# Kernel tuning notes

Measured on AMD Instinct MI355X. Metric: run time of the kernel, lower is better.

## Reference

```python
import jax, jax.numpy as jnp
import numpy as np
from jax import lax
from jax.scipy.special import logsumexp

B, T, H, L = 64, 512, 768, 9


def setup_inputs() -> dict:
    key = jax.random.key(0)
    k1, k2, k3, k4, k5 = jax.random.split(key, 5)
    hidden = jax.random.normal(k1, (B, T, H), dtype=jnp.float32)
    W = jax.random.normal(k2, (L, H), dtype=jnp.float32) * 0.02
    b = jnp.zeros((L,), dtype=jnp.float32)
    transitions = jax.random.normal(k3, (L, L), dtype=jnp.float32) * 0.1
    lengths = jax.random.randint(k4, (B,), T // 2, T + 1)
    seq_mask = jnp.arange(T)[None, :] < lengths[:, None]          # [B,T] bool
    labels = jax.random.randint(k5, (B, T), 0, L).astype(jnp.int32)
    labels = jnp.where(seq_mask, labels, -100).astype(jnp.int32)   # -100 = ignore
    attention_mask = seq_mask.astype(jnp.int32)
    return {"hidden": hidden, "W": W, "b": b, "transitions": transitions,
            "labels": labels, "attention_mask": attention_mask}


def _crf_nll(logits, tags, transitions, mask):
    # numerator: joint score of the gold path (no start/end transitions)
    maskf = mask.astype(logits.dtype)
    emit = jnp.take_along_axis(logits, tags[..., None], axis=2)[..., 0]   # [B,T]
    emit_score = (emit * maskf).sum(-1)
    trans = transitions[tags[:, :-1], tags[:, 1:]]                        # [B,T-1]
    trans_score = (trans * maskf[:, 1:]).sum(-1)
    numerator = emit_score + trans_score
    # denominator: forward algorithm (log-sum-exp recurrence over time)
    def step(alpha, xs):
        logit_t, mask_t = xs                                   # [B,L], [B]
        inner = alpha[:, :, None] + transitions[None, :, :] + logit_t[:, None, :]
        new = logsumexp(inner, axis=1)
        return jnp.where(mask_t[:, None], new, alpha), None
    alpha0 = logits[:, 0]                                      # mask[:,0] assumed True
    alpha, _ = lax.scan(step, alpha0,
                        (jnp.transpose(logits[:, 1:], (1, 0, 2)), mask[:, 1:].T))
    denominator = logsumexp(alpha, axis=-1)
    return -(numerator - denominator).sum()


def _viterbi(logits, transitions, mask):
    num_tags = transitions.shape[0]
    identity_bp = jnp.broadcast_to(jnp.arange(num_tags)[None, :], logits.shape[:1] + (num_tags,))

    def vstep(vscore, xs):
        logit_t, mask_t = xs
        inner = vscore[:, :, None] + transitions[None, :, :]   # [B,L_prev,L_cur]
        bp = jnp.argmax(inner, axis=1)                         # [B,L]
        new = jnp.max(inner, axis=1) + logit_t
        vscore = jnp.where(mask_t[:, None], new, vscore)
        bp = jnp.where(mask_t[:, None], bp, identity_bp)       # carry tag through pad
        return vscore, bp

    vscore0 = logits[:, 0]
    vscore, bps = lax.scan(vstep, vscore0,
                           (jnp.transpose(logits[:, 1:], (1, 0, 2)), mask[:, 1:].T))
    last_tag = jnp.argmax(vscore, axis=-1)                     # [B]

    def btstep(tag, bp_t):
        prev = jnp.take_along_axis(bp_t, tag[:, None], axis=1)[:, 0]
        return prev, tag

    first_tag, tags_rest = lax.scan(btstep, last_tag, bps, reverse=True)  # ys[t]=tag_{t+1}
    return jnp.concatenate([first_tag[:, None], tags_rest.T], axis=1)     # [B,T]


def reference(hidden, W, b, transitions, labels, attention_mask):
    mask = (attention_mask != 0) & (labels != -100)            # create_combined_mask
    logits = jnp.einsum('bth,lh->btl', hidden, W) + b          # classifier (dropout=eval)
    tags = jnp.where(labels == -100, 0, labels)                # adjust_labels_for_crf
    loss = _crf_nll(logits, tags, transitions, mask)           # -log_likelihood (summed)
    vtags = _viterbi(logits, transitions, mask)                # [B,T]
    # pad_predictions: prepend -100, shift right, -100 outside the masked span
    bsz = hidden.shape[0]
    neg = jnp.full((bsz, 1), -100, dtype=jnp.int32)
    shifted = jnp.concatenate([neg, vtags[:, :-1].astype(jnp.int32)], axis=1)
    valid = jnp.concatenate([jnp.zeros((bsz, 1), bool), mask[:, :-1]], axis=1)
    predictions = jnp.where(valid, shifted, -100)
    return loss, predictions
```

## Files before the change

kernel.cpp:

```cpp
#include <hip/hip_runtime.h>

#define BATCH 64
#define TLEN  512
#define HDIM  768
#define LTAGS 9

#define WS_LOGD 0
#define WS_VM   2359296
#define WS_AM   5308416
#define WS_NUM  5971968

__global__ __launch_bounds__(256) void logits_kernel(
    const float* __restrict__ hidden, const float* __restrict__ W,
    const float* __restrict__ bvec, double* __restrict__ logitsD)
{
    __shared__ float sW[LTAGS * HDIM];
    __shared__ float sb[LTAGS];
    const int tid = threadIdx.x;
    for (int i = tid; i < LTAGS * HDIM; i += 256) sW[i] = W[i];
    if (tid < LTAGS) sb[tid] = bvec[tid];
    __syncthreads();

    const int lane = tid & 63;
    const int wave = tid >> 6;
    const int sub  = lane & 7;
    const int rg   = lane >> 3;

    const int rowBase = blockIdx.x * 64 + wave * 16;
    const int r0 = rowBase + rg;
    const int r1 = rowBase + rg + 8;
    const float* h0p = hidden + (size_t)r0 * HDIM;
    const float* h1p = hidden + (size_t)r1 * HDIM;

    double acc0[LTAGS], acc1[LTAGS];
    #pragma unroll
    for (int l = 0; l < LTAGS; ++l) { acc0[l] = 0.0; acc1[l] = 0.0; }

    #pragma unroll 2
    for (int i = 0; i < 24; ++i) {
        const int off = i * 32 + sub * 4;
        const float4 h0 = *(const float4*)(h0p + off);
        const float4 h1 = *(const float4*)(h1p + off);
        #pragma unroll
        for (int l = 0; l < LTAGS; ++l) {
            const float4 w = *(const float4*)&sW[l * HDIM + off];
            float d0 = h0.x * w.x;
            d0 = fmaf(h0.y, w.y, d0); d0 = fmaf(h0.z, w.z, d0); d0 = fmaf(h0.w, w.w, d0);
            float d1 = h1.x * w.x;
            d1 = fmaf(h1.y, w.y, d1); d1 = fmaf(h1.z, w.z, d1); d1 = fmaf(h1.w, w.w, d1);
            acc0[l] += (double)d0;
            acc1[l] += (double)d1;
        }
    }
    #pragma unroll
    for (int l = 0; l < LTAGS; ++l) {
        double v0 = acc0[l], v1 = acc1[l];
        #pragma unroll
        for (int off = 4; off > 0; off >>= 1) {
            v0 += __shfl_down(v0, off);
            v1 += __shfl_down(v1, off);
        }
        acc0[l] = v0; acc1[l] = v1;
    }
    if (sub == 0) {
        #pragma unroll
        for (int l = 0; l < LTAGS; ++l) {
            logitsD[(size_t)r0 * LTAGS + l] = acc0[l] + (double)sb[l];
            logitsD[(size_t)r1 * LTAGS + l] = acc1[l] + (double)sb[l];
        }
    }
}

__global__ __launch_bounds__(256) void chunk_kernel(
    const float* __restrict__ trans, const int* __restrict__ labels,
    const int* __restrict__ att, const double* __restrict__ logitsD,
    double* __restrict__ wsVM, float* __restrict__ wsAM,
    double* __restrict__ wsNum, float* __restrict__ out)
{
    __shared__ __align__(16) double sT64[90];
    __shared__ __align__(16) float  sE32[108];
    const int tid = threadIdx.x;
    if (tid < 81) {
        const int k = tid / 9, j = tid - 9 * k;
        float tv = trans[tid];
        sT64[k * 10 + j] = (double)tv;
        sE32[k * 12 + j] = __expf(tv);
    }
    if (blockIdx.x == 0 && tid == 0) out[0] = 0.f;
    __syncthreads();

    const int blk = blockIdx.x;
    if (blk < 144) {
        const int gid = blk * 256 + tid;
        const int b   = gid / 576;
        const int rem = gid - b * 576;
        const int c   = rem / 9;
        const int i   = rem - c * 9;

        double M[LTAGS];
        #pragma unroll
        for (int j = 0; j < LTAGS; ++j) M[j] = (i == j) ? 0.0 : -1e300;

        const double* lrow = logitsD + ((size_t)b * TLEN + (c * 8 + 1)) * LTAGS;
        const int* lab = labels + b * TLEN;
        const int* am  = att + b * TLEN;
        const int t0 = c * 8 + 1;

        double lg[LTAGS], lgN[LTAGS];
        #pragma unroll
        for (int j = 0; j < LTAGS; ++j) lg[j] = lrow[j];
        bool mk = (am[t0] != 0) && (lab[t0] != -100);

        for (int s = 0; s < 8; ++s) {
            bool mkN = false;
            const int tn = t0 + s + 1;
            if (s < 7 && tn <= TLEN - 1) {
                const double* ln = lrow + (s + 1) * LTAGS;
                #pragma unroll
                for (int j = 0; j < LTAGS; ++j) lgN[j] = ln[j];
                mkN = (am[tn] != 0) && (lab[tn] != -100);
            }
            double nw[LTAGS];
            #pragma unroll
            for (int k = 0; k < LTAGS; ++k) {
                const double2* r = (const double2*)&sT64[k * 10];
                const double2 r01 = r[0], r23 = r[1], r45 = r[2], r67 = r[3];
                const double r8 = sT64[k * 10 + 8];
                const double mk64 = M[k];
                if (k == 0) {
                    nw[0] = mk64 + r01.x; nw[1] = mk64 + r01.y;
                    nw[2] = mk64 + r23.x; nw[3] = mk64 + r23.y;
                    nw[4] = mk64 + r45.x; nw[5] = mk64 + r45.y;
                    nw[6] = mk64 + r67.x; nw[7] = mk64 + r67.y;
                    nw[8] = mk64 + r8;
                } else {
                    nw[0] = fmax(nw[0], mk64 + r01.x); nw[1] = fmax(nw[1], mk64 + r01.y);
                    nw[2] = fmax(nw[2], mk64 + r23.x); nw[3] = fmax(nw[3], mk64 + r23.y);
                    nw[4] = fmax(nw[4], mk64 + r45.x); nw[5] = fmax(nw[5], mk64 + r45.y);
                    nw[6] = fmax(nw[6], mk64 + r67.x); nw[7] = fmax(nw[7], mk64 + r67.y);
                    nw[8] = fmax(nw[8], mk64 + r8);
                }
            }
            #pragma unroll
            for (int j = 0; j < LTAGS; ++j) {
                M[j] = mk ? (nw[j] + lg[j]) : M[j];
                lg[j] = lgN[j];
            }
            mk = mkN;
        }
        double* dst = wsVM + ((size_t)b * 64 + c) * 90 + (size_t)i * 10;
        #pragma unroll
        for (int j = 0; j < LTAGS; ++j) dst[j] = M[j];
    } else if (blk < 216) {
        const int gid = (blk - 144) * 256 + tid;
        const int b   = gid / 288;
        const int rem = gid - b * 288;
        const int c   = rem / 9;
        const int i   = rem - c * 9;

        float M[LTAGS];
        #pragma unroll
        for (int j = 0; j < LTAGS; ++j) M[j] = (i == j) ? 0.f : -1e30f;

        const double* lrow = logitsD + ((size_t)b * TLEN + (c * 16 + 1)) * LTAGS;
        const int* lab = labels + b * TLEN;
        const int* am  = att + b * TLEN;
        const int t0 = c * 16 + 1;

        float lg[LTAGS], lgN[LTAGS];
        #pragma unroll
        for (int j = 0; j < LTAGS; ++j) lg[j] = (float)lrow[j];
        bool mk = (am[t0] != 0) && (lab[t0] != -100);

        for (int s = 0; s < 16; ++s) {
            bool mkN = false;
            const int tn = t0 + s + 1;
            if (s < 15 && tn <= TLEN - 1) {
                const double* ln = lrow + (s + 1) * LTAGS;
                #pragma unroll
                for (int j = 0; j < LTAGS; ++j) lgN[j] = (float)ln[j];
                mkN = (am[tn] != 0) && (lab[tn] != -100);
            }
            float m = M[0];
            #pragma unroll
            for (int k = 1; k < LTAGS; ++k) m = fmaxf(m, M[k]);
            float P[LTAGS];
            #pragma unroll
            for (int k = 0; k < LTAGS; ++k) P[k] = __expf(M[k] - m);
            float sa[LTAGS];
            #pragma unroll
            for (int k = 0; k < LTAGS; ++k) {
                const float4* r = (const float4*)&sE32[k * 12];
                const float4 f03 = r[0], f47 = r[1];
                const float f8 = sE32[k * 12 + 8];
                const float pk = P[k];
                if (k == 0) {
                    sa[0] = pk * f03.x; sa[1] = pk * f03.y; sa[2] = pk * f03.z; sa[3] = pk * f03.w;
                    sa[4] = pk * f47.x; sa[5] = pk * f47.y; sa[6] = pk * f47.z; sa[7] = pk * f47.w;
                    sa[8] = pk * f8;
                } else {
                    sa[0] = fmaf(pk, f03.x, sa[0]); sa[1] = fmaf(pk, f03.y, sa[1]);
                    sa[2] = fmaf(pk, f03.z, sa[2]); sa[3] = fmaf(pk, f03.w, sa[3]);
                    sa[4] = fmaf(pk, f47.x, sa[4]); sa[5] = fmaf(pk, f47.y, sa[5]);
                    sa[6] = fmaf(pk, f47.z, sa[6]); sa[7] = fmaf(pk, f47.w, sa[7]);
                    sa[8] = fmaf(pk, f8,    sa[8]);
                }
            }
            #pragma unroll
            for (int j = 0; j < LTAGS; ++j) {
                float nwj = m + __logf(sa[j]) + lg[j];
                M[j] = mk ? nwj : M[j];
                lg[j] = lgN[j];
            }
            mk = mkN;
        }
        float* dst = wsAM + (((size_t)b * 32 + c) * LTAGS + i) * LTAGS;
        #pragma unroll
        for (int j = 0; j < LTAGS; ++j) dst[j] = M[j];
    } else {
        const int bb   = (blk - 216) * 4 + (tid >> 6);
        const int lane = tid & 63;
        const int* lab = labels + bb * TLEN;
        const int* am  = att + bb * TLEN;
        const double* lrowb = logitsD + (size_t)bb * TLEN * LTAGS;
        double part = 0.0;
        #pragma unroll
        for (int k = 0; k < 8; ++k) {
            const int t = lane + k * 64;
            int lv = lab[t], av = am[t];
            bool mkc = (av != 0) && (lv != -100);
            int tg = (lv == -100) ? 0 : lv;
            if (mkc) part += lrowb[(size_t)t * LTAGS + tg];
            if (t < TLEN - 1) {
                int lv2 = lab[t + 1], av2 = am[t + 1];
                bool mk2 = (av2 != 0) && (lv2 != -100);
                int tg2 = (lv2 == -100) ? 0 : lv2;
                if (mk2) part += sT64[tg * 10 + tg2];
            }
        }
        #pragma unroll
        for (int off = 32; off > 0; off >>= 1) part += __shfl_down(part, off);
        if (lane == 0) wsNum[bb] = part;
    }
}

__global__ __launch_bounds__(128) void crf2_kernel(
    const float* __restrict__ trans, const int* __restrict__ labels,
    const int* __restrict__ att, const double* __restrict__ logitsD,
    const double* __restrict__ wsVM, const float* __restrict__ wsAM,
    const double* __restrict__ wsNum, float* __restrict__ out)
{
    __shared__ __align__(16) double sVM[64 * 90];
    __shared__ __align__(16) float  sAM[32 * 81];
    __shared__ __align__(16) double sU[720];
    __shared__ __align__(16) double sT64[90];
    __shared__ unsigned char sMk[513];
    __shared__ int sTagB[65];
    __shared__ double sDen;

    const int b = blockIdx.x, tid = threadIdx.x;
    const int wave = tid >> 6, lane = tid & 63;
    const unsigned long long IDMAP = 0x876543210ull;

    const double2* gVM = (const double2*)(wsVM + (size_t)b * 5760);
    double2* sVM2 = (double2*)sVM;
    for (int i = tid; i < 2880; i += 128) sVM2[i] = gVM[i];
    const float4* gAM = (const float4*)(wsAM + (size_t)b * 2592);
    float4* sAM4 = (float4*)sAM;
    for (int i = tid; i < 648; i += 128) sAM4[i] = gAM[i];

    const int* lab = labels + b * TLEN;
    const int* am  = att + b * TLEN;
    for (int t = tid; t < TLEN; t += 128) {
        int lv = lab[t], av = am[t];
        sMk[t] = (av != 0 && lv != -100) ? 1 : 0;
    }
    if (tid == 0) sMk[TLEN] = 0;
    if (tid < 81) {
        const int k = tid / 9, j = tid - 9 * k;
        sT64[k * 10 + j] = (double)trans[tid];
    }
    __syncthreads();

    double* sSM = sU;
    if (tid < 72) {
        const int g = tid / 9, i = tid - 9 * g;
        double P[LTAGS];
        {
            const double* row = &sVM[(g * 8) * 90 + i * 10];
            #pragma unroll
            for (int j = 0; j < LTAGS; ++j) P[j] = row[j];
        }
        for (int m = g * 8 + 1; m < g * 8 + 8; ++m) {
            double np[LTAGS];
            #pragma unroll
            for (int k = 0; k < LTAGS; ++k) {
                const double2* r = (const double2*)&sVM[m * 90 + k * 10];
                const double2 r01 = r[0], r23 = r[1], r45 = r[2], r67 = r[3];
                const double r8 = sVM[m * 90 + k * 10 + 8];
                const double pk = P[k];
                if (k == 0) {
                    np[0] = pk + r01.x; np[1] = pk + r01.y;
                    np[2] = pk + r23.x; np[3] = pk + r23.y;
                    np[4] = pk + r45.x; np[5] = pk + r45.y;
                    np[6] = pk + r67.x; np[7] = pk + r67.y;
                    np[8] = pk + r8;
                } else {
                    np[0] = fmax(np[0], pk + r01.x); np[1] = fmax(np[1], pk + r01.y);
                    np[2] = fmax(np[2], pk + r23.x); np[3] = fmax(np[3], pk + r23.y);
                    np[4] = fmax(np[4], pk + r45.x); np[5] = fmax(np[5], pk + r45.y);
                    np[6] = fmax(np[6], pk + r67.x); np[7] = fmax(np[7], pk + r67.y);
                    np[8] = fmax(np[8], pk + r8);
                }
            }
            #pragma unroll
            for (int j = 0; j < LTAGS; ++j) P[j] = np[j];
        }
        double* dst = &sSM[g * 90 + i * 10];
        #pragma unroll
        for (int j = 0; j < LTAGS; ++j) dst[j] = P[j];
    }
    __syncthreads();

    unsigned long long* sBPp = (unsigned long long*)sU;
    unsigned long long S = IDMAP;
    int lastTag = 0;

    if (wave == 0) {
        const int c = lane;
        const int myg = c >> 3;
        double v[LTAGS], vS[LTAGS];
        #pragma unroll
        for (int j = 0; j < LTAGS; ++j) v[j] = logitsD[(size_t)b * TLEN * LTAGS + j];

        #pragma unroll
        for (int g = 0; g < 8; ++g) {
            if (g == myg) {
                #pragma unroll
                for (int j = 0; j < LTAGS; ++j) vS[j] = v[j];
            }
            double nv[LTAGS];
            #pragma unroll
            for (int k = 0; k < LTAGS; ++k) {
                const double2* r = (const double2*)&sSM[g * 90 + k * 10];
                const double2 r01 = r[0], r23 = r[1], r45 = r[2], r67 = r[3];
                const double r8 = sSM[g * 90 + k * 10 + 8];
                const double vk = v[k];
                if (k == 0) {
                    nv[0] = vk + r01.x; nv[1] = vk + r01.y;
                    nv[2] = vk + r23.x; nv[3] = vk + r23.y;
                    nv[4] = vk + r45.x; nv[5] = vk + r45.y;
                    nv[6] = vk + r67.x; nv[7] = vk + r67.y;
                    nv[8] = vk + r8;
                } else {
                    nv[0] = fmax(nv[0], vk + r01.x); nv[1] = fmax(nv[1], vk + r01.y);
                    nv[2] = fmax(nv[2], vk + r23.x); nv[3] = fmax(nv[3], vk + r23.y);
                    nv[4] = fmax(nv[4], vk + r45.x); nv[5] = fmax(nv[5], vk + r45.y);
                    nv[6] = fmax(nv[6], vk + r67.x); nv[7] = fmax(nv[7], vk + r67.y);
                    nv[8] = fmax(nv[8], vk + r8);
                }
            }
            #pragma unroll
            for (int j = 0; j < LTAGS; ++j) v[j] = nv[j];
        }
        {
            int bi = 0; double bv = v[0];
            #pragma unroll
            for (int i = 1; i < LTAGS; ++i) if (v[i] > bv) { bv = v[i]; bi = i; }
            lastTag = bi;
        }

        const int nCat = c & 7;
        for (int it = 0; it < nCat; ++it) {
            const int m = (c & ~7) + it;
            double nv[LTAGS];
            #pragma unroll
            for (int k = 0; k < LTAGS; ++k) {
                const double2* r = (const double2*)&sVM[m * 90 + k * 10];
                const double2 r01 = r[0], r23 = r[1], r45 = r[2], r67 = r[3];
                const double r8 = sVM[m * 90 + k * 10 + 8];
                const double vk = vS[k];
                if (k == 0) {
                    nv[0] = vk + r01.x; nv[1] = vk + r01.y;
                    nv[2] = vk + r23.x; nv[3] = vk + r23.y;
                    nv[4] = vk + r45.x; nv[5] = vk + r45.y;
                    nv[6] = vk + r67.x; nv[7] = vk + r67.y;
                    nv[8] = vk + r8;
                } else {
                    nv[0] = fmax(nv[0], vk + r01.x); nv[1] = fmax(nv[1], vk + r01.y);
                    nv[2] = fmax(nv[2], vk + r23.x); nv[3] = fmax(nv[3], vk + r23.y);
                    nv[4] = fmax(nv[4], vk + r45.x); nv[5] = fmax(nv[5], vk + r45.y);
                    nv[6] = fmax(nv[6], vk + r67.x); nv[7] = fmax(nv[7], vk + r67.y);
                    nv[8] = fmax(nv[8], vk + r8);
                }
            }
            #pragma unroll
            for (int j = 0; j < LTAGS; ++j) vS[j] = nv[j];
        }

        const double* lrow = logitsD + ((size_t)b * TLEN + (c * 8 + 1)) * LTAGS;
        double lg[LTAGS], lgN[LTAGS];
        #pragma unroll
        for (int j = 0; j < LTAGS; ++j) lg[j] = lrow[j];

        for (int s = 0; s < 8; ++s) {
            const int t = c * 8 + 1 + s;
            if (s < 7 && t + 1 <= TLEN - 1) {
                const double* ln = lrow + (s + 1) * LTAGS;
                #pragma unroll
                for (int j = 0; j < LTAGS; ++j) lgN[j] = ln[j];
            }
            const bool mk = (sMk[t] != 0);
            double bst[LTAGS];
            int bi[LTAGS];
            #pragma unroll
            for (int k = 0; k < LTAGS; ++k) {
                const double2* r = (const double2*)&sT64[k * 10];
                const double2 r01 = r[0], r23 = r[1], r45 = r[2], r67 = r[3];
                const double r8 = sT64[k * 10 + 8];
                const double vk = vS[k];
                double cnd[LTAGS];
                cnd[0] = vk + r01.x; cnd[1] = vk + r01.y;
                cnd[2] = vk + r23.x; cnd[3] = vk + r23.y;
                cnd[4] = vk + r45.x; cnd[5] = vk + r45.y;
                cnd[6] = vk + r67.x; cnd[7] = vk + r67.y;
                cnd[8] = vk + r8;
                if (k == 0) {
                    #pragma unroll
                    for (int j = 0; j < LTAGS; ++j) { bst[j] = cnd[j]; bi[j] = 0; }
                } else {
                    #pragma unroll
                    for (int j = 0; j < LTAGS; ++j) {
                        bool gt = cnd[j] > bst[j];
                        bst[j] = gt ? cnd[j] : bst[j];
                        bi[j]  = gt ? k : bi[j];
                    }
                }
            }
            unsigned long long pk = 0;
            #pragma unroll
            for (int j = 0; j < LTAGS; ++j)
                pk |= ((unsigned long long)bi[j]) << (4 * j);
            pk = mk ? pk : IDMAP;
            sBPp[t] = pk;
            #pragma unroll
            for (int j = 0; j < LTAGS; ++j) {
                vS[j] = mk ? (bst[j] + lg[j]) : vS[j];
                lg[j] = lgN[j];
            }
        }
        unsigned long long G = IDMAP;
        for (int s = 7; s >= 0; --s) {
            const unsigned long long bp = sBPp[c * 8 + 1 + s];
            unsigned long long ng = 0;
            #pragma unroll
            for (int j = 0; j < LTAGS; ++j) {
                int gj = (int)((G >> (4 * j)) & 15);
                int f  = (int)((bp >> (4 * gj)) & 15);
                ng |= ((unsigned long long)f) << (4 * j);
            }
            G = ng;
        }
        S = G;
    } else {
        const int j = (lane < LTAGS) ? lane : (LTAGS - 1);
        float v = (float)logitsD[(size_t)b * TLEN * LTAGS + j];
        float Mc[LTAGS], Mn[LTAGS];
        #pragma unroll
        for (int i = 0; i < LTAGS; ++i) Mc[i] = sAM[i * LTAGS + j];
        for (int c = 0; c < 32; ++c) {
            if (c < 31) {
                #pragma unroll
                for (int i = 0; i < LTAGS; ++i) Mn[i] = sAM[(c + 1) * 81 + i * LTAGS + j];
            }
            float g[LTAGS];
            #pragma unroll
            for (int i = 0; i < LTAGS; ++i) g[i] = __shfl(v, i);
            float a[LTAGS];
            #pragma unroll
            for (int i = 0; i < LTAGS; ++i) a[i] = g[i] + Mc[i];
            float t01 = fmaxf(a[0], a[1]), t23 = fmaxf(a[2], a[3]);
            float t45 = fmaxf(a[4], a[5]), t67 = fmaxf(a[6], a[7]);
            float m = fmaxf(fmaxf(fmaxf(t01, t23), fmaxf(t45, t67)), a[8]);
            float sacc = 0.f;
            #pragma unroll
            for (int i = 0; i < LTAGS; ++i) sacc += __expf(a[i] - m);
            v = m + __logf(sacc);
            if (c < 31) {
                #pragma unroll
                for (int i = 0; i < LTAGS; ++i) Mc[i] = Mn[i];
            }
        }
        float g[LTAGS];
        #pragma unroll
        for (int i = 0; i < LTAGS; ++i) g[i] = __shfl(v, i);
        if (lane == 0) {
            float m = g[0];
            #pragma unroll
            for (int i = 1; i < LTAGS; ++i) m = fmaxf(m, g[i]);
            float sacc = 0.f;
            #pragma unroll
            for (int i = 0; i < LTAGS; ++i) sacc += __expf(g[i] - m);
            sDen = (double)(m + __logf(sacc));
        }
    }

    #pragma unroll
    for (int d = 1; d < 64; d <<= 1) {
        unsigned long long Sn = __shfl_down(S, d);
        if (wave == 0 && lane + d < 64) {
            unsigned long long R = 0;
            #pragma unroll
            for (int x = 0; x < LTAGS; ++x) {
                int y = (int)((Sn >> (4 * x)) & 15);
                int z = (int)((S >> (4 * y)) & 15);
                R |= ((unsigned long long)z) << (4 * x);
            }
            S = R;
        }
    }
    if (wave == 0) {
        sTagB[tid] = (int)((S >> (4 * lastTag)) & 15);
        if (tid == 0) sTagB[64] = lastTag;
    }
    __syncthreads();

    if (tid < 64) {
        const int c = tid;
        int cur = sTagB[c + 1];
        float* po = out + 1 + b * TLEN;
        for (int s = 8; s >= 1; --s) {
            const int t = c * 8 + s;
            if (t < TLEN) {
                int nxt = (int)((sBPp[t] >> (4 * cur)) & 15);
                po[t] = sMk[t - 1] ? (float)nxt : -100.f;
                cur = nxt;
            }
        }
    }
    if (tid == 0) {
        out[1 + b * TLEN] = -100.f;
        atomicAdd(out, (float)(sDen - wsNum[b]));
    }
}

extern "C" void kernel_launch(void* const* d_in, const int* in_sizes, int n_in,
                              void* d_out, int out_size, void* d_ws, size_t ws_size,
                              hipStream_t stream)
{
    const float* hidden = (const float*)d_in[0];
    const float* W      = (const float*)d_in[1];
    const float* bvec   = (const float*)d_in[2];
    const float* trans  = (const float*)d_in[3];
    const int*   labels = (const int*)d_in[4];
    const int*   att    = (const int*)d_in[5];
    float* out = (float*)d_out;

    char* ws = (char*)d_ws;
    double* logitsD = (double*)(ws + WS_LOGD);
    double* wsVM    = (double*)(ws + WS_VM);
    float*  wsAM    = (float*)(ws + WS_AM);
    double* wsNum   = (double*)(ws + WS_NUM);

    logits_kernel<<<512, 256, 0, stream>>>(hidden, W, bvec, logitsD);
    chunk_kernel<<<232, 256, 0, stream>>>(trans, labels, att, logitsD,
                                          wsVM, wsAM, wsNum, out);
    crf2_kernel<<<BATCH, 128, 0, stream>>>(trans, labels, att, logitsD,
                                           wsVM, wsAM, wsNum, out);
}
```

Before: 221.2 us.

## Repartition chunk kernel into 512 per-batch-slice blocks with split numerator

The chunk kernel now launches 512 blocks. Each block handles one batch row and one eighth of the time axis, and runs the Viterbi chunk, logsumexp chunk and numerator work inside different wave ranges of the same block. The logits kernel uses the same swizzled block-to-row mapping, and it now zeroes the output. The numerator is split into 8 partial sums per batch that the final kernel adds up. The aim is more parallelism and better cache locality between the two kernels. The cost is many idle threads per block, since only 72, 36 and 64 lanes do work.

```diff
diff --git a/kernel.cpp b/kernel.cpp
--- a/kernel.cpp
+++ b/kernel.cpp
@@ -8,17 +8,20 @@
 #define WS_LOGD 0
 #define WS_VM   2359296
 #define WS_AM   5308416
-#define WS_NUM  5971968
+#define WS_NUMP 5971968
+
 
 __global__ __launch_bounds__(256) void logits_kernel(
     const float* __restrict__ hidden, const float* __restrict__ W,
-    const float* __restrict__ bvec, double* __restrict__ logitsD)
+    const float* __restrict__ bvec, double* __restrict__ logitsD,
+    float* __restrict__ out)
 {
     __shared__ float sW[LTAGS * HDIM];
     __shared__ float sb[LTAGS];
     const int tid = threadIdx.x;
     for (int i = tid; i < LTAGS * HDIM; i += 256) sW[i] = W[i];
     if (tid < LTAGS) sb[tid] = bvec[tid];
+    if (blockIdx.x == 0 && tid == 0) out[0] = 0.f;
     __syncthreads();
 
     const int lane = tid & 63;
@@ -26,7 +29,12 @@
     const int sub  = lane & 7;
     const int rg   = lane >> 3;
 
-    const int rowBase = blockIdx.x * 64 + wave * 16;
+    const int B   = blockIdx.x;
+    const int res = B & 7, mq = B >> 3;
+    const int b   = ((mq >> 3) << 3) + res;
+    const int jw  = mq & 7;
+
+    const int rowBase = b * TLEN + jw * 64 + wave * 16;
     const int r0 = rowBase + rg;
     const int r1 = rowBase + rg + 8;
     const float* h0p = hidden + (size_t)r0 * HDIM;
@@ -75,7 +83,7 @@
     const float* __restrict__ trans, const int* __restrict__ labels,
     const int* __restrict__ att, const double* __restrict__ logitsD,
     double* __restrict__ wsVM, float* __restrict__ wsAM,
-    double* __restrict__ wsNum, float* __restrict__ out)
+    double* __restrict__ wsNumP)
 {
     __shared__ __align__(16) double sT64[90];
     __shared__ __align__(16) float  sE32[108];
@@ -86,24 +94,25 @@
         sT64[k * 10 + j] = (double)tv;
         sE32[k * 12 + j] = __expf(tv);
     }
-    if (blockIdx.x == 0 && tid == 0) out[0] = 0.f;
     __syncthreads();
 
-    const int blk = blockIdx.x;
-    if (blk < 144) {
-        const int gid = blk * 256 + tid;
-        const int b   = gid / 576;
-        const int rem = gid - b * 576;
-        const int c   = rem / 9;
-        const int i   = rem - c * 9;
+    const int B   = blockIdx.x;
+    const int res = B & 7, mq = B >> 3;
+    const int b   = ((mq >> 3) << 3) + res;
+    const int jw  = mq & 7;
+
+    const int* lab = labels + b * TLEN;
+    const int* am  = att + b * TLEN;
+
+    if (tid < 72) {
+        const int cl = tid / 9, i = tid - 9 * cl;
+        const int c  = jw * 8 + cl;
 
         double M[LTAGS];
         #pragma unroll
         for (int j = 0; j < LTAGS; ++j) M[j] = (i == j) ? 0.0 : -1e300;
 
         const double* lrow = logitsD + ((size_t)b * TLEN + (c * 8 + 1)) * LTAGS;
-        const int* lab = labels + b * TLEN;
-        const int* am  = att + b * TLEN;
         const int t0 = c * 8 + 1;
 
         double lg[LTAGS], lgN[LTAGS];
@@ -151,20 +160,16 @@
         double* dst = wsVM + ((size_t)b * 64 + c) * 90 + (size_t)i * 10;
         #pragma unroll
         for (int j = 0; j < LTAGS; ++j) dst[j] = M[j];
-    } else if (blk < 216) {
-        const int gid = (blk - 144) * 256 + tid;
-        const int b   = gid / 288;
-        const int rem = gid - b * 288;
-        const int c   = rem / 9;
-        const int i   = rem - c * 9;
+    } else if (tid >= 128 && tid < 164) {
+        const int idx = tid - 128;
+        const int cl = idx / 9, i = idx - 9 * cl;
+        const int c  = jw * 4 + cl;
 
         float M[LTAGS];
         #pragma unroll
         for (int j = 0; j < LTAGS; ++j) M[j] = (i == j) ? 0.f : -1e30f;
 
         const double* lrow = logitsD + ((size_t)b * TLEN + (c * 16 + 1)) * LTAGS;
-        const int* lab = labels + b * TLEN;
-        const int* am  = att + b * TLEN;
         const int t0 = c * 16 + 1;
 
         float lg[LTAGS], lgN[LTAGS];
@@ -217,16 +222,12 @@
         float* dst = wsAM + (((size_t)b * 32 + c) * LTAGS + i) * LTAGS;
         #pragma unroll
         for (int j = 0; j < LTAGS; ++j) dst[j] = M[j];
-    } else {
-        const int bb   = (blk - 216) * 4 + (tid >> 6);
-        const int lane = tid & 63;
-        const int* lab = labels + bb * TLEN;
-        const int* am  = att + bb * TLEN;
-        const double* lrowb = logitsD + (size_t)bb * TLEN * LTAGS;
+    } else if (tid >= 192) {
+        const int lane = tid - 192;
+        const int t = jw * 64 + lane;
+        const double* lrowb = logitsD + (size_t)b * TLEN * LTAGS;
         double part = 0.0;
-        #pragma unroll
-        for (int k = 0; k < 8; ++k) {
-            const int t = lane + k * 64;
+        {
             int lv = lab[t], av = am[t];
             bool mkc = (av != 0) && (lv != -100);
             int tg = (lv == -100) ? 0 : lv;
@@ -240,7 +241,7 @@
         }
         #pragma unroll
         for (int off = 32; off > 0; off >>= 1) part += __shfl_down(part, off);
-        if (lane == 0) wsNum[bb] = part;
+        if (lane == 0) wsNumP[b * 8 + jw] = part;
     }
 }
 
@@ -248,7 +249,7 @@
     const float* __restrict__ trans, const int* __restrict__ labels,
     const int* __restrict__ att, const double* __restrict__ logitsD,
     const double* __restrict__ wsVM, const float* __restrict__ wsAM,
-    const double* __restrict__ wsNum, float* __restrict__ out)
+    const double* __restrict__ wsNumP, float* __restrict__ out)
 {
     __shared__ __align__(16) double sVM[64 * 90];
     __shared__ __align__(16) float  sAM[32 * 81];
@@ -540,7 +541,11 @@
     }
     if (tid == 0) {
         out[1 + b * TLEN] = -100.f;
-        atomicAdd(out, (float)(sDen - wsNum[b]));
+        double num = 0.0;
+        const double* np = wsNumP + b * 8;
+        #pragma unroll
+        for (int q = 0; q < 8; ++q) num += np[q];
+        atomicAdd(out, (float)(sDen - num));
     }
 }
 
@@ -560,11 +565,11 @@
     double* logitsD = (double*)(ws + WS_LOGD);
     double* wsVM    = (double*)(ws + WS_VM);
     float*  wsAM    = (float*)(ws + WS_AM);
-    double* wsNum   = (double*)(ws + WS_NUM);
-
-    logits_kernel<<<512, 256, 0, stream>>>(hidden, W, bvec, logitsD);
-    chunk_kernel<<<232, 256, 0, stream>>>(trans, labels, att, logitsD,
-                                          wsVM, wsAM, wsNum, out);
+    double* wsNumP  = (double*)(ws + WS_NUMP);
+
+    logits_kernel<<<512, 256, 0, stream>>>(hidden, W, bvec, logitsD, out);
+    chunk_kernel<<<512, 256, 0, stream>>>(trans, labels, att, logitsD,
+                                          wsVM, wsAM, wsNumP);
     crf2_kernel<<<BATCH, 128, 0, stream>>>(trans, labels, att, logitsD,
-                                           wsVM, wsAM, wsNum, out);
+                                           wsVM, wsAM, wsNumP, out);
 }
```

Result: no change. 219.2 us (-0.9%).
